# Optimization experiments

Hardware: AMD Instinct MI355X
Metric: run time of the kernel (lower is better)

The kernel has to match this reference:

```python
import jax, jax.numpy as jnp
import numpy as np

N = 50000
NEG_SLOPE = 0.2  # PyG GATConv default
EPS = 1e-16      # PyG softmax denominator epsilon


def gat_conv(x, src, dst, W, a_src, a_dst, b):
    """Single-head PyG-style GATConv. src/dst already include self-loops."""
    h = x @ W                                   # [N, out]
    alpha_s = h @ a_src                         # [N]
    alpha_d = h @ a_dst                         # [N]
    e = alpha_s[src] + alpha_d[dst]             # [E]
    e = jnp.where(e >= 0, e, NEG_SLOPE * e)     # LeakyReLU
    # segment softmax over incoming edges of each dst node
    m = jax.ops.segment_max(e, dst, num_segments=N)
    ex = jnp.exp(e - m[dst])
    denom = jax.ops.segment_sum(ex, dst, num_segments=N)
    alpha = ex / (denom[dst] + EPS)             # [E]
    out = jax.ops.segment_sum(h[src] * alpha[:, None], dst, num_segments=N)
    return out + b


def add_self_loops(edge_index):
    loop = jnp.arange(N, dtype=edge_index.dtype)
    src = jnp.concatenate([edge_index[0], loop])
    dst = jnp.concatenate([edge_index[1], loop])
    return src, dst


def setup_inputs() -> dict:
    key = jax.random.key(0)
    ks = jax.random.split(key, 10)
    F_in, H, C, E = 128, 128, 16, 800000
    x = jax.random.normal(ks[0], (N, F_in), dtype=jnp.float32)
    edge_index = jax.random.randint(ks[1], (2, E), 0, N, dtype=jnp.int64)
    s1 = 1.0 / np.sqrt(F_in)
    s2 = 1.0 / np.sqrt(H)
    W1 = jax.random.uniform(ks[2], (F_in, H), jnp.float32, -s1, s1)
    a_src1 = jax.random.uniform(ks[3], (H,), jnp.float32, -s2, s2)
    a_dst1 = jax.random.uniform(ks[4], (H,), jnp.float32, -s2, s2)
    b1 = jnp.zeros((H,), jnp.float32)
    W2 = jax.random.uniform(ks[5], (H, C), jnp.float32, -s2, s2)
    sc = 1.0 / np.sqrt(C)
    a_src2 = jax.random.uniform(ks[6], (C,), jnp.float32, -sc, sc)
    a_dst2 = jax.random.uniform(ks[7], (C,), jnp.float32, -sc, sc)
    b2 = jnp.zeros((C,), jnp.float32)
    return {"x": x, "edge_index": edge_index, "W1": W1, "a_src1": a_src1,
            "a_dst1": a_dst1, "b1": b1, "W2": W2, "a_src2": a_src2,
            "a_dst2": a_dst2, "b2": b2}


def reference(x, edge_index, W1, a_src1, a_dst1, b1, W2, a_src2, a_dst2, b2):
    src, dst = add_self_loops(edge_index)
    h = gat_conv(x, src, dst, W1, a_src1, a_dst1, b1)
    h = jax.nn.relu(h)
    # dropout is identity at inference (droprate applied only in training)
    out = gat_conv(h, src, dst, W2, a_src2, a_dst2, b2)
    return jax.nn.log_softmax(out, axis=1)
```

## Files before the change

kernel.cpp:

```cpp
#include <hip/hip_runtime.h>
#include <math.h>

#define NODES 50000
#define NEDGE 800000
#define ETOT  (NEDGE + NODES)
#define CAP   96
#define GBLK  ((NODES + 31) / 32)
#define BSH   10
#define NBUCK ((NODES + 1023) / 1024)
#define BCAP  24576
#define SCAP  20480

typedef unsigned short ushort_t;
typedef unsigned int uint_t;

__device__ __forceinline__ ushort_t f2bf(float f) {
    uint_t u = __float_as_uint(f);
    return (ushort_t)((u + 0x7fffu + ((u >> 16) & 1u)) >> 16);
}

__global__ void gemm_xw_alpha(const float* __restrict__ X, const float* __restrict__ W,
                              const float* __restrict__ a_src, const float* __restrict__ a_dst,
                              ushort_t* __restrict__ Hb, float* __restrict__ as_,
                              float* __restrict__ ad_, int n) {
    __shared__ float xs[32][132];
    const int t = threadIdx.x;
    const int ct = t & 31;
    const int rg = t >> 5;
    const int row0 = blockIdx.x * 32;
    #pragma unroll
    for (int i = 0; i < 16; ++i) {
        int idx = i * 256 + t;
        int r = idx >> 7, c = idx & 127;
        int row = row0 + r;
        xs[r][c] = (row < n) ? X[(size_t)row * 128 + c] : 0.f;
    }
    __syncthreads();
    float acc[4][4];
    #pragma unroll
    for (int r = 0; r < 4; ++r)
        #pragma unroll
        for (int c = 0; c < 4; ++c) acc[r][c] = 0.f;

    const float* Wp = W + 4 * ct;
    for (int k4 = 0; k4 < 32; ++k4) {
        float4 w0 = *(const float4*)(Wp + (size_t)(k4 * 4 + 0) * 128);
        float4 w1 = *(const float4*)(Wp + (size_t)(k4 * 4 + 1) * 128);
        float4 w2 = *(const float4*)(Wp + (size_t)(k4 * 4 + 2) * 128);
        float4 w3 = *(const float4*)(Wp + (size_t)(k4 * 4 + 3) * 128);
        float4 xv[4];
        #pragma unroll
        for (int r = 0; r < 4; ++r)
            xv[r] = *(const float4*)(&xs[rg * 4 + r][k4 * 4]);
        #pragma unroll
        for (int r = 0; r < 4; ++r) {
            acc[r][0] += xv[r].x * w0.x + xv[r].y * w1.x + xv[r].z * w2.x + xv[r].w * w3.x;
            acc[r][1] += xv[r].x * w0.y + xv[r].y * w1.y + xv[r].z * w2.y + xv[r].w * w3.y;
            acc[r][2] += xv[r].x * w0.z + xv[r].y * w1.z + xv[r].z * w2.z + xv[r].w * w3.z;
            acc[r][3] += xv[r].x * w0.w + xv[r].y * w1.w + xv[r].z * w2.w + xv[r].w * w3.w;
        }
    }
    const float4 asv = *(const float4*)(a_src + 4 * ct);
    const float4 adv = *(const float4*)(a_dst + 4 * ct);
    #pragma unroll
    for (int r = 0; r < 4; ++r) {
        int row = row0 + rg * 4 + r;
        bool ok = row < n;
        if (ok) {
            uint_t lo = (uint_t)f2bf(acc[r][0]) | ((uint_t)f2bf(acc[r][1]) << 16);
            uint_t hi = (uint_t)f2bf(acc[r][2]) | ((uint_t)f2bf(acc[r][3]) << 16);
            uint2 pk; pk.x = lo; pk.y = hi;
            *(uint2*)(Hb + (size_t)row * 128 + 4 * ct) = pk;
        }
        float s = acc[r][0] * asv.x + acc[r][1] * asv.y + acc[r][2] * asv.z + acc[r][3] * asv.w;
        float d = acc[r][0] * adv.x + acc[r][1] * adv.y + acc[r][2] * adv.z + acc[r][3] * adv.w;
        #pragma unroll
        for (int off = 16; off; off >>= 1) {
            s += __shfl_down(s, off, 32);
            d += __shfl_down(d, off, 32);
        }
        if (ct == 0 && ok) { as_[row] = s; ad_[row] = d; }
    }
}

__global__ void bin_pass1(const int* __restrict__ ei, int* __restrict__ bcnt,
                          uint_t* __restrict__ packed) {
    __shared__ int lh[NBUCK];
    __shared__ int gbase_[NBUCK];
    const int t = threadIdx.x;
    const int e0 = blockIdx.x * 1024;
    if (t < NBUCK) lh[t] = 0;
    __syncthreads();
    int s[4], d[4], bk[4];
    const int eb = e0 + 4 * t;
    if (eb + 3 < NEDGE) {
        int4 sv = *(const int4*)(ei + eb);
        int4 dv = *(const int4*)(ei + NEDGE + eb);
        s[0] = sv.x; s[1] = sv.y; s[2] = sv.z; s[3] = sv.w;
        d[0] = dv.x; d[1] = dv.y; d[2] = dv.z; d[3] = dv.w;
        #pragma unroll
        for (int j = 0; j < 4; ++j) bk[j] = d[j] >> BSH;
    } else {
        #pragma unroll
        for (int j = 0; j < 4; ++j) {
            int e = eb + j;
            if (e >= ETOT) { bk[j] = -1; }
            else if (e < NEDGE) { s[j] = ei[e]; d[j] = ei[NEDGE + e]; bk[j] = d[j] >> BSH; }
            else { s[j] = d[j] = e - NEDGE; bk[j] = d[j] >> BSH; }
        }
    }
    #pragma unroll
    for (int j = 0; j < 4; ++j)
        if (bk[j] >= 0) atomicAdd(&lh[bk[j]], 1);
    __syncthreads();
    if (t < NBUCK) {
        int c = lh[t];
        gbase_[t] = c ? atomicAdd(&bcnt[t], c) : 0;
        lh[t] = 0;
    }
    __syncthreads();
    #pragma unroll
    for (int j = 0; j < 4; ++j) {
        if (bk[j] >= 0) {
            int lpos = atomicAdd(&lh[bk[j]], 1);
            int pos = gbase_[bk[j]] + lpos;
            if (pos < BCAP)
                packed[(size_t)bk[j] * BCAP + pos] = ((uint_t)d[j] << 16) | (uint_t)s[j];
        }
    }
}

__global__ void bin_pass2(const int* __restrict__ bcnt, const uint_t* __restrict__ packed,
                          int* __restrict__ rowptr, ushort_t* __restrict__ srcs) {
    __shared__ ushort_t sbuf[SCAP];
    __shared__ int lcnt[1024], lexc[1024];
    __shared__ int wsum[4];
    __shared__ int gbs_s;
    const int t = threadIdx.x;
    const int b = blockIdx.x;
    const int n0 = b << BSH;
    const int nEnd = (n0 + 1024 < NODES) ? n0 + 1024 : NODES;
    const int cnt = bcnt[b];
    const uint_t* pk = packed + (size_t)b * BCAP;
    if (t < 64) {
        int c = (t < NBUCK) ? bcnt[t] : 0;
        int sv = c;
        #pragma unroll
        for (int off = 1; off < 64; off <<= 1) {
            int o = __shfl_up(sv, off);
            if (t >= off) sv += o;
        }
        if (t == b) gbs_s = sv - c;
    }
    for (int i = t; i < 1024; i += 256) lcnt[i] = 0;
    __syncthreads();
    for (int i = t; i < cnt; i += 256) {
        int dl = (int)(pk[i] >> 16) - n0;
        atomicAdd(&lcnt[dl], 1);
    }
    __syncthreads();
    int c0 = lcnt[4 * t], c1 = lcnt[4 * t + 1], c2 = lcnt[4 * t + 2], c3 = lcnt[4 * t + 3];
    int s4 = c0 + c1 + c2 + c3;
    int lane = t & 63, wv = t >> 6;
    int sv = s4;
    #pragma unroll
    for (int off = 1; off < 64; off <<= 1) {
        int o = __shfl_up(sv, off);
        if (lane >= off) sv += o;
    }
    if (lane == 63) wsum[wv] = sv;
    __syncthreads();
    int add = 0;
    for (int j = 0; j < wv; ++j) add += wsum[j];
    int base = add + sv - s4;
    lexc[4 * t]     = base;
    lexc[4 * t + 1] = base + c0;
    lexc[4 * t + 2] = base + c0 + c1;
    lexc[4 * t + 3] = base + c0 + c1 + c2;
    const int gb = gbs_s;
    #pragma unroll
    for (int j = 0; j < 4; ++j) {
        int n = n0 + 4 * t + j;
        if (n < nEnd) rowptr[n] = gb + lexc[4 * t + j];
    }
    if (b == NBUCK - 1 && t == 255) rowptr[NODES] = gb + cnt;
    __syncthreads();
    for (int i = t; i < 1024; i += 256) lcnt[i] = lexc[i];
    __syncthreads();
    if (cnt <= SCAP) {
        for (int i = t; i < cnt; i += 256) {
            uint_t e = pk[i];
            int dl = (int)(e >> 16) - n0;
            int lp = atomicAdd(&lcnt[dl], 1);
            sbuf[lp] = (ushort_t)(e & 0xffffu);
        }
        __syncthreads();
        for (int i = t; i < cnt; i += 256)
            srcs[(size_t)gb + i] = sbuf[i];
    } else {
        for (int i = t; i < cnt; i += 256) {
            uint_t e = pk[i];
            int dl = (int)(e >> 16) - n0;
            int lp = atomicAdd(&lcnt[dl], 1);
            srcs[(size_t)gb + lp] = (ushort_t)(e & 0xffffu);
        }
    }
}

__global__ void gat_fused128(const int* __restrict__ rowptr, const ushort_t* __restrict__ srcs,
                             const float* __restrict__ as_, const float* __restrict__ ad_,
                             const ushort_t* __restrict__ Hb, const float* __restrict__ b,
                             ushort_t* __restrict__ outb) {
    __shared__ float sw[4][CAP];
    __shared__ int   ss[4][CAP];
    int wid = (blockIdx.x * blockDim.x + threadIdx.x) >> 6;
    int lane = threadIdx.x & 63;
    int wv = (threadIdx.x >> 6) & 3;
    if (wid >= NODES) return;
    const int beg = rowptr[wid], deg = rowptr[wid + 1] - beg;
    const float adv = ad_[wid];
    float den = 0.f;
    for (int i = lane; i < deg; i += 64) {
        int s = srcs[beg + i];
        float v = as_[s] + adv;
        v = (v >= 0.f) ? v : 0.2f * v;
        float w = __expf(v);
        if (i < CAP) { sw[wv][i] = w; ss[wv][i] = s; }
        den += w;
    }
    #pragma unroll
    for (int off = 32; off; off >>= 1) den += __shfl_xor(den, off);
    const float invd = 1.f / (den + 1e-16f);
    float ax = 0.f, ay = 0.f;
    const int nl = deg < CAP ? deg : CAP;
    int i = 0;
    for (; i + 4 <= nl; i += 4) {
        float w0 = sw[wv][i], w1 = sw[wv][i + 1], w2 = sw[wv][i + 2], w3 = sw[wv][i + 3];
        int s0 = ss[wv][i], s1 = ss[wv][i + 1], s2 = ss[wv][i + 2], s3 = ss[wv][i + 3];
        uint_t u0 = *(const uint_t*)(Hb + (size_t)s0 * 128 + lane * 2);
        uint_t u1 = *(const uint_t*)(Hb + (size_t)s1 * 128 + lane * 2);
        uint_t u2 = *(const uint_t*)(Hb + (size_t)s2 * 128 + lane * 2);
        uint_t u3 = *(const uint_t*)(Hb + (size_t)s3 * 128 + lane * 2);
        ax += w0 * __uint_as_float(u0 << 16) + w1 * __uint_as_float(u1 << 16)
            + w2 * __uint_as_float(u2 << 16) + w3 * __uint_as_float(u3 << 16);
        ay += w0 * __uint_as_float(u0 & 0xffff0000u) + w1 * __uint_as_float(u1 & 0xffff0000u)
            + w2 * __uint_as_float(u2 & 0xffff0000u) + w3 * __uint_as_float(u3 & 0xffff0000u);
    }
    for (; i < nl; ++i) {
        float w0 = sw[wv][i];
        int s0 = ss[wv][i];
        uint_t u0 = *(const uint_t*)(Hb + (size_t)s0 * 128 + lane * 2);
        ax += w0 * __uint_as_float(u0 << 16);
        ay += w0 * __uint_as_float(u0 & 0xffff0000u);
    }
    for (int j = CAP; j < deg; ++j) {
        int s0 = srcs[beg + j];
        float v = as_[s0] + adv; v = (v >= 0.f) ? v : 0.2f * v;
        float w0 = __expf(v);
        uint_t u0 = *(const uint_t*)(Hb + (size_t)s0 * 128 + lane * 2);
        ax += w0 * __uint_as_float(u0 << 16);
        ay += w0 * __uint_as_float(u0 & 0xffff0000u);
    }
    float ox = fmaxf(ax * invd + b[lane * 2], 0.f);
    float oy = fmaxf(ay * invd + b[lane * 2 + 1], 0.f);
    uint_t pk = (uint_t)f2bf(ox) | ((uint_t)f2bf(oy) << 16);
    *(uint_t*)(outb + (size_t)wid * 128 + lane * 2) = pk;
}

__global__ void gemm_hw2_alpha(const ushort_t* __restrict__ Hinb, const float* __restrict__ W,
                               const float* __restrict__ a_src, const float* __restrict__ a_dst,
                               float* __restrict__ Hout, float* __restrict__ as_,
                               float* __restrict__ ad_, int n) {
    __shared__ float wl[128 * 16];
    for (int i = threadIdx.x; i < 128 * 16; i += 256) wl[i] = W[i];
    __syncthreads();
    int tid = blockIdx.x * blockDim.x + threadIdx.x;
    int node = tid >> 4, col = tid & 15;
    if (node >= n) return;
    const uint4* hr = (const uint4*)(Hinb + (size_t)node * 128);
    float acc = 0.f;
    #pragma unroll
    for (int i = 0; i < 16; ++i) {
        uint4 q = hr[i];
        int k = i * 8;
        acc += __uint_as_float(q.x << 16)          * wl[(k + 0) * 16 + col];
        acc += __uint_as_float(q.x & 0xffff0000u)  * wl[(k + 1) * 16 + col];
        acc += __uint_as_float(q.y << 16)          * wl[(k + 2) * 16 + col];
        acc += __uint_as_float(q.y & 0xffff0000u)  * wl[(k + 3) * 16 + col];
        acc += __uint_as_float(q.z << 16)          * wl[(k + 4) * 16 + col];
        acc += __uint_as_float(q.z & 0xffff0000u)  * wl[(k + 5) * 16 + col];
        acc += __uint_as_float(q.w << 16)          * wl[(k + 6) * 16 + col];
        acc += __uint_as_float(q.w & 0xffff0000u)  * wl[(k + 7) * 16 + col];
    }
    Hout[(size_t)node * 16 + col] = acc;
    float ps = acc * a_src[col], pd = acc * a_dst[col];
    #pragma unroll
    for (int off = 1; off < 16; off <<= 1) {
        ps += __shfl_xor(ps, off);
        pd += __shfl_xor(pd, off);
    }
    if (col == 0) { as_[node] = ps; ad_[node] = pd; }
}

__global__ void gat_fused16_lsm(const int* __restrict__ rowptr, const ushort_t* __restrict__ srcs,
                                const float* __restrict__ as_, const float* __restrict__ ad_,
                                const float* __restrict__ H, const float* __restrict__ b,
                                float* __restrict__ out) {
    __shared__ float sw[4][CAP];
    __shared__ int   ss[4][CAP];
    int wid = (blockIdx.x * blockDim.x + threadIdx.x) >> 6;
    int lane = threadIdx.x & 63;
    int wv = (threadIdx.x >> 6) & 3;
    int slot = lane >> 4, k = lane & 15;
    if (wid >= NODES) return;
    const int beg = rowptr[wid], deg = rowptr[wid + 1] - beg;
    const float adv = ad_[wid];
    float den = 0.f;
    for (int i = lane; i < deg; i += 64) {
        int s = srcs[beg + i];
        float v = as_[s] + adv;
        v = (v >= 0.f) ? v : 0.2f * v;
        float w = __expf(v);
        if (i < CAP) { sw[wv][i] = w; ss[wv][i] = s; }
        den += w;
    }
    #pragma unroll
    for (int off = 32; off; off >>= 1) den += __shfl_xor(den, off);
    const float invd = 1.f / (den + 1e-16f);
    float acc = 0.f;
    const int nl = deg < CAP ? deg : CAP;
    for (int i = slot; i < nl; i += 4) {
        acc += sw[wv][i] * H[(size_t)ss[wv][i] * 16 + k];
    }
    for (int j = CAP + slot; j < deg; j += 4) {
        int s = srcs[beg + j];
        float v = as_[s] + adv; v = (v >= 0.f) ? v : 0.2f * v;
        acc += __expf(v) * H[(size_t)s * 16 + k];
    }
    acc += __shfl_xor(acc, 16);
    acc += __shfl_xor(acc, 32);
    float v = acc * invd + b[k];
    float mx = v;
    #pragma unroll
    for (int off = 1; off < 16; off <<= 1) mx = fmaxf(mx, __shfl_xor(mx, off));
    float ex = __expf(v - mx), ssum = ex;
    #pragma unroll
    for (int off = 1; off < 16; off <<= 1) ssum += __shfl_xor(ssum, off);
    float r = v - mx - __logf(ssum);
    if (lane < 16) out[(size_t)wid * 16 + k] = r;
}

extern "C" void kernel_launch(void* const* d_in, const int* in_sizes, int n_in,
                              void* d_out, int out_size, void* d_ws, size_t ws_size,
                              hipStream_t stream) {
    const float* x      = (const float*)d_in[0];
    const int*   ei     = (const int*)d_in[1];
    const float* W1     = (const float*)d_in[2];
    const float* a_src1 = (const float*)d_in[3];
    const float* a_dst1 = (const float*)d_in[4];
    const float* b1     = (const float*)d_in[5];
    const float* W2     = (const float*)d_in[6];
    const float* a_src2 = (const float*)d_in[7];
    const float* a_dst2 = (const float*)d_in[8];
    const float* b2     = (const float*)d_in[9];
    float* out = (float*)d_out;

    float* p = (float*)d_ws;
    ushort_t* h1b   = (ushort_t*)p; p += (size_t)NODES * 64;
    ushort_t* agg1b = (ushort_t*)p; p += (size_t)NODES * 64;
    float* h2     = p; p += (size_t)NODES * 16;
    float* as_    = p; p += NODES;
    float* ad_    = p; p += NODES;
    float* as2    = p; p += NODES;
    float* ad2    = p; p += NODES;
    uint_t* packed = (uint_t*)p; p += (size_t)NBUCK * BCAP;
    int* ip = (int*)p;
    int* rowptr = ip; ip += NODES + 1;
    int* bcnt   = ip; ip += 64;
    ushort_t* srcs = (ushort_t*)ip;

    const int WAVEGRID = (NODES * 64 + 255) / 256;

    hipMemsetAsync(bcnt, 0, 64 * sizeof(int), stream);
    bin_pass1<<<(ETOT + 1023) / 1024, 256, 0, stream>>>(ei, bcnt, packed);
    bin_pass2<<<NBUCK, 256, 0, stream>>>(bcnt, packed, rowptr, srcs);

    gemm_xw_alpha<<<GBLK, 256, 0, stream>>>(x, W1, a_src1, a_dst1, h1b, as_, ad_, NODES);
    gat_fused128<<<WAVEGRID, 256, 0, stream>>>(rowptr, srcs, as_, ad_, h1b, b1, agg1b);

    gemm_hw2_alpha<<<(NODES * 16 + 255) / 256, 256, 0, stream>>>(agg1b, W2, a_src2, a_dst2, h2, as2, ad2, NODES);
    gat_fused16_lsm<<<WAVEGRID, 256, 0, stream>>>(rowptr, srcs, as2, ad2, h2, b2, out);
}
```

Measured before the change: 177.3 us.

## Compute layer-1 XW projection with bf16 MFMA instead of scalar FP32 FMAs

Rewrites the first-layer GEMM kernel to use the 16x16x32 bf16 MFMA instruction. W is staged transposed into shared memory as bf16, and each wave converts its X rows to bf16 fragments. Each block now handles 64 rows instead of 32. The attention dot products are reduced from the MFMA accumulator layout with xor-shuffles. This lowers the compute cost of the projection but rounds X and W to bf16 before multiplying, and H stores become scalar 2-byte writes.

```diff
diff --git a/kernel.cpp b/kernel.cpp
--- a/kernel.cpp
+++ b/kernel.cpp
@@ -5,7 +5,8 @@
 #define NEDGE 800000
 #define ETOT  (NEDGE + NODES)
 #define CAP   96
-#define GBLK  ((NODES + 31) / 32)
+#define GROWS 64
+#define GBLK  ((NODES + GROWS - 1) / GROWS)
 #define BSH   10
 #define NBUCK ((NODES + 1023) / 1024)
 #define BCAP  24576
@@ -13,73 +14,89 @@
 
 typedef unsigned short ushort_t;
 typedef unsigned int uint_t;
+typedef __attribute__((ext_vector_type(8))) short bf16x8;
+typedef __attribute__((ext_vector_type(4))) float f32x4;
 
 __device__ __forceinline__ ushort_t f2bf(float f) {
     uint_t u = __float_as_uint(f);
     return (ushort_t)((u + 0x7fffu + ((u >> 16) & 1u)) >> 16);
+}
+__device__ __forceinline__ uint_t pack2bf(float a, float b) {
+    return (uint_t)f2bf(a) | ((uint_t)f2bf(b) << 16);
 }
 
 __global__ void gemm_xw_alpha(const float* __restrict__ X, const float* __restrict__ W,
                               const float* __restrict__ a_src, const float* __restrict__ a_dst,
                               ushort_t* __restrict__ Hb, float* __restrict__ as_,
                               float* __restrict__ ad_, int n) {
-    __shared__ float xs[32][132];
+    __shared__ __align__(16) ushort_t wt[128][136];
+    __shared__ float asl[128], adl[128];
     const int t = threadIdx.x;
-    const int ct = t & 31;
-    const int rg = t >> 5;
-    const int row0 = blockIdx.x * 32;
     #pragma unroll
     for (int i = 0; i < 16; ++i) {
         int idx = i * 256 + t;
-        int r = idx >> 7, c = idx & 127;
-        int row = row0 + r;
-        xs[r][c] = (row < n) ? X[(size_t)row * 128 + c] : 0.f;
-    }
-    __syncthreads();
-    float acc[4][4];
-    #pragma unroll
-    for (int r = 0; r < 4; ++r)
-        #pragma unroll
-        for (int c = 0; c < 4; ++c) acc[r][c] = 0.f;
-
-    const float* Wp = W + 4 * ct;
-    for (int k4 = 0; k4 < 32; ++k4) {
-        float4 w0 = *(const float4*)(Wp + (size_t)(k4 * 4 + 0) * 128);
-        float4 w1 = *(const float4*)(Wp + (size_t)(k4 * 4 + 1) * 128);
-        float4 w2 = *(const float4*)(Wp + (size_t)(k4 * 4 + 2) * 128);
-        float4 w3 = *(const float4*)(Wp + (size_t)(k4 * 4 + 3) * 128);
-        float4 xv[4];
-        #pragma unroll
-        for (int r = 0; r < 4; ++r)
-            xv[r] = *(const float4*)(&xs[rg * 4 + r][k4 * 4]);
-        #pragma unroll
-        for (int r = 0; r < 4; ++r) {
-            acc[r][0] += xv[r].x * w0.x + xv[r].y * w1.x + xv[r].z * w2.x + xv[r].w * w3.x;
-            acc[r][1] += xv[r].x * w0.y + xv[r].y * w1.y + xv[r].z * w2.y + xv[r].w * w3.y;
-            acc[r][2] += xv[r].x * w0.z + xv[r].y * w1.z + xv[r].z * w2.z + xv[r].w * w3.z;
-            acc[r][3] += xv[r].x * w0.w + xv[r].y * w1.w + xv[r].z * w2.w + xv[r].w * w3.w;
-        }
-    }
-    const float4 asv = *(const float4*)(a_src + 4 * ct);
-    const float4 adv = *(const float4*)(a_dst + 4 * ct);
+        int k = idx >> 5, c4 = (idx & 31) * 4;
+        float4 w = *(const float4*)(W + (size_t)k * 128 + c4);
+        wt[c4 + 0][k] = f2bf(w.x);
+        wt[c4 + 1][k] = f2bf(w.y);
+        wt[c4 + 2][k] = f2bf(w.z);
+        wt[c4 + 3][k] = f2bf(w.w);
+    }
+    if (t < 128) { asl[t] = a_src[t]; adl[t] = a_dst[t]; }
+    __syncthreads();
+
+    const int lane = t & 63, wid = t >> 6;
+    const int r0 = blockIdx.x * GROWS + wid * 16;
+    const int arow = r0 + (lane & 15);
+    const int kq = (lane >> 4) * 8;
+
+    bf16x8 afrag[4];
+    #pragma unroll
+    for (int ks = 0; ks < 4; ++ks) {
+        union { bf16x8 v; uint_t u[4]; } af;
+        if (arow < n) {
+            const float* xp = X + (size_t)arow * 128 + ks * 32 + kq;
+            float4 xa = *(const float4*)(xp);
+            float4 xb = *(const float4*)(xp + 4);
+            af.u[0] = pack2bf(xa.x, xa.y); af.u[1] = pack2bf(xa.z, xa.w);
+            af.u[2] = pack2bf(xb.x, xb.y); af.u[3] = pack2bf(xb.z, xb.w);
+        } else {
+            af.u[0] = af.u[1] = af.u[2] = af.u[3] = 0u;
+        }
+        afrag[ks] = af.v;
+    }
+
+    f32x4 acc[8];
+    #pragma unroll
+    for (int c = 0; c < 8; ++c) { acc[c].x = 0.f; acc[c].y = 0.f; acc[c].z = 0.f; acc[c].w = 0.f; }
+    #pragma unroll
+    for (int c = 0; c < 8; ++c) {
+        #pragma unroll
+        for (int ks = 0; ks < 4; ++ks) {
+            const bf16x8 bfrag = *(const bf16x8*)(&wt[c * 16 + (lane & 15)][ks * 32 + kq]);
+            acc[c] = __builtin_amdgcn_mfma_f32_16x16x32_bf16(afrag[ks], bfrag, acc[c], 0, 0, 0);
+        }
+    }
+
+    const int q = lane >> 4, cl = lane & 15;
     #pragma unroll
     for (int r = 0; r < 4; ++r) {
-        int row = row0 + rg * 4 + r;
+        int row = r0 + q * 4 + r;
         bool ok = row < n;
-        if (ok) {
-            uint_t lo = (uint_t)f2bf(acc[r][0]) | ((uint_t)f2bf(acc[r][1]) << 16);
-            uint_t hi = (uint_t)f2bf(acc[r][2]) | ((uint_t)f2bf(acc[r][3]) << 16);
-            uint2 pk; pk.x = lo; pk.y = hi;
-            *(uint2*)(Hb + (size_t)row * 128 + 4 * ct) = pk;
-        }
-        float s = acc[r][0] * asv.x + acc[r][1] * asv.y + acc[r][2] * asv.z + acc[r][3] * asv.w;
-        float d = acc[r][0] * adv.x + acc[r][1] * adv.y + acc[r][2] * adv.z + acc[r][3] * adv.w;
-        #pragma unroll
-        for (int off = 16; off; off >>= 1) {
-            s += __shfl_down(s, off, 32);
-            d += __shfl_down(d, off, 32);
-        }
-        if (ct == 0 && ok) { as_[row] = s; ad_[row] = d; }
+        float s = 0.f, d = 0.f;
+        #pragma unroll
+        for (int c = 0; c < 8; ++c) {
+            float v = (r == 0) ? acc[c].x : (r == 1) ? acc[c].y : (r == 2) ? acc[c].z : acc[c].w;
+            if (ok) Hb[(size_t)row * 128 + c * 16 + cl] = f2bf(v);
+            s += v * asl[c * 16 + cl];
+            d += v * adl[c * 16 + cl];
+        }
+        #pragma unroll
+        for (int off = 1; off < 16; off <<= 1) {
+            s += __shfl_xor(s, off);
+            d += __shfl_xor(d, off);
+        }
+        if (cl == 0 && ok) { as_[row] = s; ad_[row] = d; }
     }
 }
 
@@ -180,8 +197,8 @@
     const int gb = gbs_s;
     #pragma unroll
     for (int j = 0; j < 4; ++j) {
-        int n = n0 + 4 * t + j;
-        if (n < nEnd) rowptr[n] = gb + lexc[4 * t + j];
+        int nn = n0 + 4 * t + j;
+        if (nn < nEnd) rowptr[nn] = gb + lexc[4 * t + j];
     }
     if (b == NBUCK - 1 && t == 255) rowptr[NODES] = gb + cnt;
     __syncthreads();
```

Result: faster. 158.4 us (-10.6%).
